# Optimization experiments

Hardware: AMD Instinct MI355X
Metric: run time of the kernel (lower is better)

Reference implementation:

```python
import jax, jax.numpy as jnp
from jax import lax
import numpy as np

B, N, H = 8, 2048, 128
THRESH = 0.3


def setup_inputs() -> dict:
    key = jax.random.key(0)
    k1, k2, k3 = jax.random.split(key, 3)
    node_embeddings = jax.random.normal(k1, (B * N, H), jnp.float32)
    # contiguous equal-sized graphs, as produced by PyG-style batching
    batch = jnp.repeat(jnp.arange(B, dtype=jnp.int64), N)
    # path_scorer params: Linear(2H->H) then Linear(H->1)
    W1 = jax.random.normal(k2, (2 * H, H), jnp.float32) * 0.02  # input-major
    b1 = jnp.zeros((H,), jnp.float32)
    W2 = jax.random.normal(k3, (H,), jnp.float32) * 0.02
    b2 = jnp.zeros((), jnp.float32)
    return {"node_embeddings": node_embeddings, "batch": batch,
            "W1": W1, "b1": b1, "W2": W2, "b2": b2}


def _run(emb, W1, b1, W2, b2):
    """emb: [B, N, H]. Returns (path [B,N] int32 padded with -1, scores [B,N])."""
    Bn, Nn, Hh = emb.shape
    bidx = jnp.arange(Bn)
    nidx = jnp.arange(Nn)
    # split first Linear: score(i,j) = sigmoid(w2 . elu(e_i@W1a + e_j@W1b + b1) + b2)
    A = jnp.einsum('bnh,hk->bnk', emb, W1[:Hh])          # current-node half [B,N,H]
    C = jnp.einsum('bnh,hk->bnk', emb, W1[Hh:]) + b1     # neighbor half + bias [B,N,H]
    root = jnp.argmax(emb[:, :, 0], axis=1)              # [B]
    visited0 = jnp.zeros((Bn, Nn), bool).at[bidx, root].set(True)

    def step(carry, _):
        cur, visited, active = carry
        # score every node against the current node in one fused pass
        h = jax.nn.elu(A[bidx, cur][:, None, :] + C)                      # [B,N,H]
        s = jax.nn.sigmoid(jnp.einsum('bnh,h->bn', h, W2) + b2)           # [B,N]
        sm = jnp.where(visited, -jnp.inf, s)
        best = jnp.argmax(sm, axis=1)                                     # first max == stable sort
        bscore = jnp.take_along_axis(sm, best[:, None], axis=1)[:, 0]
        take = active & (bscore > THRESH)
        visited = visited | (take[:, None] & (nidx[None, :] == best[:, None]))
        new_cur = jnp.where(take, best, cur)
        step_path = jnp.where(take, best, -1).astype(jnp.int32)
        step_score = jnp.where(take, bscore, 0.0).astype(emb.dtype)
        return (new_cur, visited, take), (step_path, step_score)

    init = (root, visited0, jnp.ones((Bn,), bool))
    _, (paths, scoreseq) = lax.scan(step, init, None, length=Nn - 1)
    path = jnp.concatenate([root[:, None].astype(jnp.int32), paths.T], axis=1)      # [B,N]
    scores = jnp.concatenate([jnp.ones((Bn, 1), emb.dtype), scoreseq.T], axis=1)    # root score = 1.0
    return path, scores


def reference(node_embeddings, batch, W1, b1, W2, b2):
    num_graphs = int(batch[-1]) + 1  # contiguous equal-sized graphs
    emb = node_embeddings.reshape(num_graphs, -1, node_embeddings.shape[-1])
    return _run(emb, W1, b1, W2, b2)
```

## Files before the change

kernel.cpp:

```cpp
#include <hip/hip_runtime.h>
#include <math.h>

#define B_ 8
#define N_ 2048
#define H_ 128
#define BN_ (B_ * N_)


typedef int i32x2 __attribute__((ext_vector_type(2)));

__device__ __forceinline__ float elu1(float x) {
    return x > 0.f ? x : (__expf(x) - 1.f);
}

__device__ __forceinline__ unsigned enc_key(float v) {
    unsigned u = __float_as_uint(v);
    return (u & 0x80000000u) ? ~u : (u | 0x80000000u);
}
__device__ __forceinline__ float dec_key(unsigned k) {
    return __uint_as_float((k & 0x80000000u) ? (k & 0x7FFFFFFFu) : ~k);
}
__device__ __forceinline__ unsigned umax2(unsigned a, unsigned b) { return a > b ? a : b; }

__device__ __forceinline__ unsigned wave_umax64(unsigned x) {
    unsigned t;
    t = (unsigned)__builtin_amdgcn_update_dpp((int)x, (int)x, 0xB1, 0xF, 0xF, false);
    x = umax2(x, t);
    t = (unsigned)__builtin_amdgcn_update_dpp((int)x, (int)x, 0x4E, 0xF, 0xF, false);
    x = umax2(x, t);
    t = (unsigned)__builtin_amdgcn_update_dpp((int)x, (int)x, 0x124, 0xF, 0xF, false);
    x = umax2(x, t);
    t = (unsigned)__builtin_amdgcn_update_dpp((int)x, (int)x, 0x128, 0xF, 0xF, false);
    x = umax2(x, t);
#if __has_builtin(__builtin_amdgcn_permlane16_swap)
    {
        i32x2 r = __builtin_amdgcn_permlane16_swap((int)x, (int)x, false, false);
        x = umax2((unsigned)r.x, (unsigned)r.y);
    }
#else
    x = umax2(x, (unsigned)__shfl_xor((int)x, 16));
#endif
#if __has_builtin(__builtin_amdgcn_permlane32_swap)
    {
        i32x2 r = __builtin_amdgcn_permlane32_swap((int)x, (int)x, false, false);
        x = umax2((unsigned)r.x, (unsigned)r.y);
    }
#else
    x = umax2(x, (unsigned)__shfl_xor((int)x, 32));
#endif
    return x;
}

__global__ __launch_bounds__(H_) void k_ac(const float* __restrict__ emb,
                                           const float* __restrict__ W1,
                                           const float* __restrict__ b1,
                                           float* __restrict__ A,
                                           float* __restrict__ C) {
    __shared__ float e[H_];
    const int i = blockIdx.x;
    const int k = threadIdx.x;
    e[k] = emb[(size_t)i * H_ + k];
    __syncthreads();
    float a = 0.f, c = 0.f;
#pragma unroll 8
    for (int h = 0; h < H_; ++h) {
        const float ev = e[h];
        a = fmaf(ev, W1[h * H_ + k], a);
        c = fmaf(ev, W1[(H_ + h) * H_ + k], c);
    }
    A[(size_t)i * H_ + k] = a;
    C[(size_t)i * H_ + k] = c + b1[k];
}

__global__ __launch_bounds__(256) void k_z(const float* __restrict__ A,
                                           const float* __restrict__ Cc,
                                           const float* __restrict__ w2,
                                           const float* __restrict__ b2p,
                                           unsigned* __restrict__ K) {
    const int lane = threadIdx.x & 63;
    const int wave = threadIdx.x >> 6;
    const int g = blockIdx.x >> 8;
    const int sub = blockIdx.x & 255;
    const int rowtile = sub & 127;
    const int jh = sub >> 7;
    const int ibase = rowtile * 16 + wave * 4;
    const int i = ibase + (lane & 3);
    const int he = (lane >> 2) * 8;
    const float b2v = *b2p;

    const float* Arow = A + ((size_t)g * N_ + i) * H_ + he;
    const float4 a0 = *(const float4*)(Arow);
    const float4 a1 = *(const float4*)(Arow + 4);
    const float4 w0 = *(const float4*)(w2 + he);
    const float4 w1v = *(const float4*)(w2 + he + 4);
    const float* Cg = Cc + (size_t)g * N_ * H_ + he;
    unsigned* Krow = K + ((size_t)g * N_ + i) * N_;
    const bool writer = ((lane >> 2) == 0);

    const int j0 = jh * 1024;
    for (int j = j0; j < j0 + 1024; j += 8) {
        float4 c0[8], c1[8];
#pragma unroll
        for (int q = 0; q < 8; ++q) {
            const float* Cj = Cg + (size_t)(j + q) * H_;
            c0[q] = *(const float4*)(Cj);
            c1[q] = *(const float4*)(Cj + 4);
        }
        float pv[8];
#pragma unroll
        for (int q = 0; q < 8; ++q) {
            float p = 0.f;
            p = fmaf(w0.x, elu1(a0.x + c0[q].x), p);
            p = fmaf(w0.y, elu1(a0.y + c0[q].y), p);
            p = fmaf(w0.z, elu1(a0.z + c0[q].z), p);
            p = fmaf(w0.w, elu1(a0.w + c0[q].w), p);
            p = fmaf(w1v.x, elu1(a1.x + c1[q].x), p);
            p = fmaf(w1v.y, elu1(a1.y + c1[q].y), p);
            p = fmaf(w1v.z, elu1(a1.z + c1[q].z), p);
            p = fmaf(w1v.w, elu1(a1.w + c1[q].w), p);
            pv[q] = p;
        }
#pragma unroll
        for (int q = 0; q < 8; ++q) pv[q] += __shfl_xor(pv[q], 4);
#pragma unroll
        for (int q = 0; q < 8; ++q) pv[q] += __shfl_xor(pv[q], 8);
#pragma unroll
        for (int q = 0; q < 8; ++q) pv[q] += __shfl_xor(pv[q], 16);
#pragma unroll
        for (int q = 0; q < 8; ++q) pv[q] += __shfl_xor(pv[q], 32);
        if (writer) {
            uint4 ka, kb;
            ka.x = enc_key(pv[0] + b2v);
            ka.y = enc_key(pv[1] + b2v);
            ka.z = enc_key(pv[2] + b2v);
            ka.w = enc_key(pv[3] + b2v);
            kb.x = enc_key(pv[4] + b2v);
            kb.y = enc_key(pv[5] + b2v);
            kb.z = enc_key(pv[6] + b2v);
            kb.w = enc_key(pv[7] + b2v);
            *(uint4*)(Krow + j) = ka;
            *(uint4*)(Krow + j + 4) = kb;
        }
    }
}

__global__ __launch_bounds__(64, 1) void k_path8(const float* __restrict__ emb,
                                                 const unsigned* __restrict__ K,
                                                 float* __restrict__ out) {
    const int g = blockIdx.x;
    const int lane = threadIdx.x;

    float bv0 = -INFINITY;
    int bi0 = 0x7fffffff;
    for (int j = lane; j < N_; j += 64) {
        const float v = emb[((size_t)g * N_ + j) * H_];
        if (v > bv0) { bv0 = v; bi0 = j; }
    }
#pragma unroll
    for (int off = 1; off < 64; off <<= 1) {
        const float ov = __shfl_xor(bv0, off);
        const int oi = __shfl_xor(bi0, off);
        if (ov > bv0 || (ov == bv0 && oi < bi0)) { bv0 = ov; bi0 = oi; }
    }
    int cur = bi0;
    unsigned vbits = 0;
    if (((cur >> 2) & 63) == lane)
        vbits |= 1u << (((cur >> 8) << 2) | (cur & 3));

    float* pathOut = out + (size_t)g * N_;
    float* scoreOut = out + (size_t)BN_ + (size_t)g * N_;
    if (lane == 0) {
        pathOut[0] = (float)cur;
        scoreOut[0] = 1.0f;
    }

    const unsigned* Kg = K + (size_t)g * N_ * N_;
    uint4 z[8];
    {
        const uint4* Kr = (const uint4*)(Kg + ((size_t)cur << 11));
#pragma unroll
        for (int k = 0; k < 8; ++k) z[k] = Kr[k * 64 + lane];
    }

    int t = 1;
    for (; t < N_; ++t) {
        unsigned kv[32];
#define MASK(S, RAW) kv[S] = (RAW) & (((vbits >> (S)) & 1u) - 1u);
        MASK(0,  z[0].x) MASK(1,  z[0].y) MASK(2,  z[0].z) MASK(3,  z[0].w)
        MASK(4,  z[1].x) MASK(5,  z[1].y) MASK(6,  z[1].z) MASK(7,  z[1].w)
        MASK(8,  z[2].x) MASK(9,  z[2].y) MASK(10, z[2].z) MASK(11, z[2].w)
        MASK(12, z[3].x) MASK(13, z[3].y) MASK(14, z[3].z) MASK(15, z[3].w)
        MASK(16, z[4].x) MASK(17, z[4].y) MASK(18, z[4].z) MASK(19, z[4].w)
        MASK(20, z[5].x) MASK(21, z[5].y) MASK(22, z[5].z) MASK(23, z[5].w)
        MASK(24, z[6].x) MASK(25, z[6].y) MASK(26, z[6].z) MASK(27, z[6].w)
        MASK(28, z[7].x) MASK(29, z[7].y) MASK(30, z[7].z) MASK(31, z[7].w)
#undef MASK

        unsigned m16[16];
#pragma unroll
        for (int i = 0; i < 16; ++i) m16[i] = umax2(kv[i], kv[i + 16]);
        unsigned m8[8];
#pragma unroll
        for (int i = 0; i < 8; ++i) m8[i] = umax2(m16[i], m16[i + 8]);
        unsigned m4[4];
#pragma unroll
        for (int i = 0; i < 4; ++i) m4[i] = umax2(m8[i], m8[i + 4]);
        const unsigned lanemax =
            umax2(umax2(m4[0], m4[1]), umax2(m4[2], m4[3]));

        const unsigned w = wave_umax64(lanemax);

        unsigned ma = 0, mb = 0, mc = 0, md = 0;
#pragma unroll
        for (int s = 0; s < 8; ++s) {
            ma |= (kv[s] == w) ? (1u << s) : 0u;
            mb |= (kv[s + 8] == w) ? (1u << (s + 8)) : 0u;
            mc |= (kv[s + 16] == w) ? (1u << (s + 16)) : 0u;
            md |= (kv[s + 24] == w) ? (1u << (s + 24)) : 0u;
        }
        const unsigned mm = (ma | mb) | (mc | md);
        const unsigned long long mk = __ballot(mm != 0u);
        int bi;
        if (__popcll(mk) == 1) {
            const int src = (int)(__ffsll((long long)mk) - 1);
            const unsigned mmw = __shfl(mm, src);
            const int slot = __ffs(mmw) - 1;
            bi = ((slot >> 2) << 8) | (src << 2) | (slot & 3);
        } else {
            unsigned cand = 0u;
            if (mm) {
                const int slot = __ffs(mm) - 1;
                cand = ~(unsigned)(((slot >> 2) << 8) | (lane << 2) | (slot & 3));
            }
#pragma unroll
            for (int off = 1; off < 64; off <<= 1) {
                const unsigned oc = __shfl_xor(cand, off);
                if (oc > cand) cand = oc;
            }
            bi = (int)(~cand);
        }

        {
            const uint4* Kr = (const uint4*)(Kg + ((size_t)bi << 11));
#pragma unroll
            for (int k = 0; k < 8; ++k) z[k] = Kr[k * 64 + lane];
        }

        const float bv = dec_key(w);
        const float s = 1.f / (1.f + expf(-bv));
        if (!((double)s > 0.3)) break;
        cur = bi;
        if (((cur >> 2) & 63) == lane)
            vbits |= 1u << (((cur >> 8) << 2) | (cur & 3));
        if (lane == 0) {
            pathOut[t] = (float)cur;
            scoreOut[t] = s;
        }
    }
    for (int tt = t + lane; tt < N_; tt += 64) {
        pathOut[tt] = -1.f;
        scoreOut[tt] = 0.f;
    }
}

__device__ __forceinline__ void blockArgmax(float& bv, int& bi, float* rv, int* ri,
                                            int lane, int wid, int nw) {
#pragma unroll
    for (int off = 1; off < 64; off <<= 1) {
        const float ov = __shfl_xor(bv, off);
        const int oi = __shfl_xor(bi, off);
        if (ov > bv || (ov == bv && oi < bi)) { bv = ov; bi = oi; }
    }
    if (lane == 0) { rv[wid] = bv; ri[wid] = bi; }
    __syncthreads();
    if (wid == 0) {
        float v = (lane < nw) ? rv[lane] : -INFINITY;
        int ix = (lane < nw) ? ri[lane] : 0x7fffffff;
#pragma unroll
        for (int off = 1; off < 16; off <<= 1) {
            const float ov = __shfl_xor(v, off);
            const int oi = __shfl_xor(ix, off);
            if (ov > v || (ov == v && oi < ix)) { v = ov; ix = oi; }
        }
        if (lane == 0) { rv[0] = v; ri[0] = ix; }
    }
    __syncthreads();
    bv = rv[0];
    bi = ri[0];
}

__global__ __launch_bounds__(1024) void k_path_fly(const float* __restrict__ emb,
                                                   const float* __restrict__ A,
                                                   const float* __restrict__ Cc,
                                                   const float* __restrict__ w2g,
                                                   const float* __restrict__ b2p,
                                                   float* __restrict__ out) {
    const int g = blockIdx.x;
    const int tid = threadIdx.x;
    const int lane = tid & 63, wid = tid >> 6;
    __shared__ float acur[H_], w2s[H_];
    __shared__ unsigned char vis[N_];
    __shared__ float rv[16];
    __shared__ int ri[16];
    const float b2v = *b2p;
    if (tid < H_) w2s[tid] = w2g[tid];
    for (int j = tid; j < N_; j += 1024) vis[j] = 0;

    float bv = -INFINITY;
    int bi = 0x7fffffff;
    for (int j = tid; j < N_; j += 1024) {
        const float v = emb[((size_t)g * N_ + j) * H_];
        if (v > bv) { bv = v; bi = j; }
    }
    __syncthreads();
    blockArgmax(bv, bi, rv, ri, lane, wid, 16);
    int cur = bi;
    float* pathOut = out + (size_t)g * N_;
    float* scoreOut = out + (size_t)BN_ + (size_t)g * N_;
    if (tid == 0) {
        vis[cur] = 1;
        pathOut[0] = (float)cur;
        scoreOut[0] = 1.0f;
    }
    __syncthreads();

    int t = 1;
    for (; t < N_; ++t) {
        if (tid < H_) acur[tid] = A[((size_t)g * N_ + cur) * H_ + tid];
        __syncthreads();
        float mbv = -INFINITY;
        int mbi = 0x7fffffff;
#pragma unroll
        for (int q = 0; q < 2; ++q) {
            const int j = tid + q * 1024;
            const float* Cj = Cc + ((size_t)g * N_ + j) * H_;
            float p = 0.f;
            for (int h = 0; h < H_; h += 4) {
                const float4 c = *(const float4*)(Cj + h);
                p = fmaf(w2s[h + 0], elu1(acur[h + 0] + c.x), p);
                p = fmaf(w2s[h + 1], elu1(acur[h + 1] + c.y), p);
                p = fmaf(w2s[h + 2], elu1(acur[h + 2] + c.z), p);
                p = fmaf(w2s[h + 3], elu1(acur[h + 3] + c.w), p);
            }
            const float z = p + b2v;
            if (!vis[j] && (z > mbv || (z == mbv && j < mbi))) { mbv = z; mbi = j; }
        }
        __syncthreads();
        blockArgmax(mbv, mbi, rv, ri, lane, wid, 16);
        const float s = 1.f / (1.f + expf(-mbv));
        if (!((double)s > 0.3)) break;
        cur = mbi;
        if (tid == 0) {
            vis[cur] = 1;
            pathOut[t] = (float)cur;
            scoreOut[t] = s;
        }
        __syncthreads();
    }
    for (int tt = t + tid; tt < N_; tt += 1024) {
        pathOut[tt] = -1.f;
        scoreOut[tt] = 0.f;
    }
}

extern "C" void kernel_launch(void* const* d_in, const int* in_sizes, int n_in,
                              void* d_out, int out_size, void* d_ws, size_t ws_size,
                              hipStream_t stream) {
    (void)in_sizes; (void)n_in; (void)out_size;
    const float* emb = (const float*)d_in[0];
    const float* W1 = (const float*)d_in[2];
    const float* b1 = (const float*)d_in[3];
    const float* w2 = (const float*)d_in[4];
    const float* b2 = (const float*)d_in[5];
    float* out = (float*)d_out;

    float* A = (float*)d_ws;
    float* C = A + (size_t)BN_ * H_;
    unsigned* K = (unsigned*)(C + (size_t)BN_ * H_);
    const size_t need = ((size_t)BN_ * H_ * 2 + (size_t)B_ * N_ * N_) * sizeof(float);

    hipLaunchKernelGGL(k_ac, dim3(BN_), dim3(H_), 0, stream, emb, W1, b1, A, C);
    if (ws_size >= need) {
        hipLaunchKernelGGL(k_z, dim3(2048), dim3(256), 0, stream, A, C, w2, b2, K);
        hipLaunchKernelGGL(k_path8, dim3(B_), dim3(64), 0, stream, emb, K, out);
    } else {
        hipLaunchKernelGGL(k_path_fly, dim3(B_), dim3(1024), 0, stream,
                           emb, A, C, w2, b2, out);
    }
}
```

Baseline: 3.071 ms.

## Tile pairwise score kernel through LDS with per-lane column ownership

Measured after the change: 4.238 ms. +38.0%, slower.

```diff
diff --git a/kernel.cpp b/kernel.cpp
--- a/kernel.cpp
+++ b/kernel.cpp
@@ -72,74 +72,84 @@
     C[(size_t)i * H_ + k] = c + b1[k];
 }
 
-__global__ __launch_bounds__(256) void k_z(const float* __restrict__ A,
-                                           const float* __restrict__ Cc,
-                                           const float* __restrict__ w2,
-                                           const float* __restrict__ b2p,
-                                           unsigned* __restrict__ K) {
-    const int lane = threadIdx.x & 63;
-    const int wave = threadIdx.x >> 6;
+__global__ __launch_bounds__(256) void k_z2(const float* __restrict__ A,
+                                            const float* __restrict__ Cc,
+                                            const float* __restrict__ w2,
+                                            const float* __restrict__ b2p,
+                                            unsigned* __restrict__ K) {
+    __shared__ float4 Cs[64 * 33];
+    __shared__ float4 Asf[512];
+    __shared__ float4 ws4[32];
+
+    const int tid = threadIdx.x;
+    const int lane = tid & 63;
+    const int wv = tid >> 6;
     const int g = blockIdx.x >> 8;
     const int sub = blockIdx.x & 255;
     const int rowtile = sub & 127;
     const int jh = sub >> 7;
-    const int ibase = rowtile * 16 + wave * 4;
-    const int i = ibase + (lane & 3);
-    const int he = (lane >> 2) * 8;
     const float b2v = *b2p;
 
-    const float* Arow = A + ((size_t)g * N_ + i) * H_ + he;
-    const float4 a0 = *(const float4*)(Arow);
-    const float4 a1 = *(const float4*)(Arow + 4);
-    const float4 w0 = *(const float4*)(w2 + he);
-    const float4 w1v = *(const float4*)(w2 + he + 4);
-    const float* Cg = Cc + (size_t)g * N_ * H_ + he;
-    unsigned* Krow = K + ((size_t)g * N_ + i) * N_;
-    const bool writer = ((lane >> 2) == 0);
-
-    const int j0 = jh * 1024;
-    for (int j = j0; j < j0 + 1024; j += 8) {
-        float4 c0[8], c1[8];
-#pragma unroll
-        for (int q = 0; q < 8; ++q) {
-            const float* Cj = Cg + (size_t)(j + q) * H_;
-            c0[q] = *(const float4*)(Cj);
-            c1[q] = *(const float4*)(Cj + 4);
-        }
-        float pv[8];
-#pragma unroll
-        for (int q = 0; q < 8; ++q) {
-            float p = 0.f;
-            p = fmaf(w0.x, elu1(a0.x + c0[q].x), p);
-            p = fmaf(w0.y, elu1(a0.y + c0[q].y), p);
-            p = fmaf(w0.z, elu1(a0.z + c0[q].z), p);
-            p = fmaf(w0.w, elu1(a0.w + c0[q].w), p);
-            p = fmaf(w1v.x, elu1(a1.x + c1[q].x), p);
-            p = fmaf(w1v.y, elu1(a1.y + c1[q].y), p);
-            p = fmaf(w1v.z, elu1(a1.z + c1[q].z), p);
-            p = fmaf(w1v.w, elu1(a1.w + c1[q].w), p);
-            pv[q] = p;
-        }
-#pragma unroll
-        for (int q = 0; q < 8; ++q) pv[q] += __shfl_xor(pv[q], 4);
-#pragma unroll
-        for (int q = 0; q < 8; ++q) pv[q] += __shfl_xor(pv[q], 8);
-#pragma unroll
-        for (int q = 0; q < 8; ++q) pv[q] += __shfl_xor(pv[q], 16);
-#pragma unroll
-        for (int q = 0; q < 8; ++q) pv[q] += __shfl_xor(pv[q], 32);
-        if (writer) {
-            uint4 ka, kb;
-            ka.x = enc_key(pv[0] + b2v);
-            ka.y = enc_key(pv[1] + b2v);
-            ka.z = enc_key(pv[2] + b2v);
-            ka.w = enc_key(pv[3] + b2v);
-            kb.x = enc_key(pv[4] + b2v);
-            kb.y = enc_key(pv[5] + b2v);
-            kb.z = enc_key(pv[6] + b2v);
-            kb.w = enc_key(pv[7] + b2v);
-            *(uint4*)(Krow + j) = ka;
-            *(uint4*)(Krow + j + 4) = kb;
+    {
+        const float4* Ag = (const float4*)(A + ((size_t)g * N_ + rowtile * 16) * H_);
+        Asf[tid] = Ag[tid];
+        Asf[tid + 256] = Ag[tid + 256];
+        if (tid < 32) ws4[tid] = ((const float4*)w2)[tid];
+    }
+
+    const int j0h = jh * 1024;
+    unsigned* Kbase = K + ((size_t)g * N_ + rowtile * 16) * N_;
+    const float* ws = (const float*)ws4;
+
+    for (int tt = 0; tt < 16; ++tt) {
+        const int j0 = j0h + tt * 64;
+        __syncthreads();
+        {
+            const float4* Cg = (const float4*)(Cc + ((size_t)g * N_ + j0) * H_);
+#pragma unroll
+            for (int q = 0; q < 8; ++q) {
+                const int idx = q * 256 + tid;
+                const int row = idx >> 5;
+                const int c4 = idx & 31;
+                Cs[row * 33 + c4] = Cg[idx];
+            }
+        }
+        __syncthreads();
+
+        const float4* Crow = &Cs[lane * 33];
+#pragma unroll
+        for (int ii = 0; ii < 4; ++ii) {
+            const int il = wv * 4 + ii;
+            const float* Ar = (const float*)&Asf[il * 32];
+            float p[16];
+#pragma unroll
+            for (int s = 0; s < 16; ++s) {
+                const float4 c0 = Crow[2 * s];
+                const float4 c1 = Crow[2 * s + 1];
+                const float4 a0 = *(const float4*)(Ar + s * 8);
+                const float4 a1 = *(const float4*)(Ar + s * 8 + 4);
+                const float4 w0 = *(const float4*)(ws + s * 8);
+                const float4 w1v = *(const float4*)(ws + s * 8 + 4);
+                float p_ = 0.f;
+                p_ = fmaf(w0.x, elu1(a0.x + c0.x), p_);
+                p_ = fmaf(w0.y, elu1(a0.y + c0.y), p_);
+                p_ = fmaf(w0.z, elu1(a0.z + c0.z), p_);
+                p_ = fmaf(w0.w, elu1(a0.w + c0.w), p_);
+                p_ = fmaf(w1v.x, elu1(a1.x + c1.x), p_);
+                p_ = fmaf(w1v.y, elu1(a1.y + c1.y), p_);
+                p_ = fmaf(w1v.z, elu1(a1.z + c1.z), p_);
+                p_ = fmaf(w1v.w, elu1(a1.w + c1.w), p_);
+                p[s] = p_;
+            }
+            float t1[8], t2[4], t3[2];
+#pragma unroll
+            for (int k = 0; k < 8; ++k) t1[k] = p[2 * k] + p[2 * k + 1];
+#pragma unroll
+            for (int k = 0; k < 4; ++k) t2[k] = t1[2 * k] + t1[2 * k + 1];
+#pragma unroll
+            for (int k = 0; k < 2; ++k) t3[k] = t2[2 * k] + t2[2 * k + 1];
+            const float z = t3[0] + t3[1];
+            Kbase[(size_t)il * N_ + j0 + lane] = enc_key(z + b2v);
         }
     }
 }
@@ -381,7 +391,7 @@
 
     hipLaunchKernelGGL(k_ac, dim3(BN_), dim3(H_), 0, stream, emb, W1, b1, A, C);
     if (ws_size >= need) {
-        hipLaunchKernelGGL(k_z, dim3(2048), dim3(256), 0, stream, A, C, w2, b2, K);
+        hipLaunchKernelGGL(k_z2, dim3(2048), dim3(256), 0, stream, A, C, w2, b2, K);
         hipLaunchKernelGGL(k_path8, dim3(B_), dim3(64), 0, stream, emb, K, out);
     } else {
         hipLaunchKernelGGL(k_path_fly, dim3(B_), dim3(1024), 0, stream,
```
